# Kernel tuning notes

Hardware: AMD Instinct MI355X
Metric: run time of the kernel (lower is better)

Reference implementation:

```python
import jax, jax.numpy as jnp
import numpy as np

D_MODEL = 1024
N_HEADS = 16
D_FF = 512  # FeedForward default d_ff=512 (not overridden in EncoderLayer)
EPS = 1e-6


def _norm(x, alpha, bias):
    # Custom NormLayer: mean + UNBIASED variance (torch.var default, N-1 denom)
    mean = jnp.mean(x, axis=-1, keepdims=True)
    n = x.shape[-1]
    var = jnp.sum((x - mean) ** 2, axis=-1, keepdims=True) / (n - 1)
    return alpha * (x - mean) / jnp.sqrt(var + EPS) + bias


def setup_inputs() -> dict:
    key = jax.random.key(0)
    ks = jax.random.split(key, 12)
    s = 1.0 / np.sqrt(D_MODEL)
    inp = {
        "x": jax.random.normal(ks[0], (2, 2048, D_MODEL), dtype=jnp.float32),
        "Wq": jax.random.uniform(ks[1], (D_MODEL, D_MODEL), jnp.float32, -s, s),
        "bq": jnp.zeros((D_MODEL,), jnp.float32),
        "Wk": jax.random.uniform(ks[2], (D_MODEL, D_MODEL), jnp.float32, -s, s),
        "bk": jnp.zeros((D_MODEL,), jnp.float32),
        "Wv": jax.random.uniform(ks[3], (D_MODEL, D_MODEL), jnp.float32, -s, s),
        "bv": jnp.zeros((D_MODEL,), jnp.float32),
        "Wo": jax.random.uniform(ks[4], (D_MODEL, D_MODEL), jnp.float32, -s, s),
        "bo": jnp.zeros((D_MODEL,), jnp.float32),
        "alpha1": jnp.ones((D_MODEL,), jnp.float32),
        "beta1": jnp.zeros((D_MODEL,), jnp.float32),
        "alpha2": jnp.ones((D_MODEL,), jnp.float32),
        "beta2": jnp.zeros((D_MODEL,), jnp.float32),
        "W1": jax.random.uniform(ks[5], (D_MODEL, D_FF), jnp.float32, -s, s),
        "b1": jnp.zeros((D_FF,), jnp.float32),
        "W2": jax.random.uniform(ks[6], (D_FF, D_MODEL), jnp.float32, -1.0 / np.sqrt(D_FF), 1.0 / np.sqrt(D_FF)),
        "b2": jnp.zeros((D_MODEL,), jnp.float32),
    }
    return inp


def reference(x, Wq, bq, Wk, bk, Wv, bv, Wo, bo, alpha1, beta1, alpha2, beta2, W1, b1, W2, b2):
    B, S, D = x.shape
    H = N_HEADS
    dh = D // H
    # norm_1 applied to x, result feeds BOTH attention and the residual
    x = _norm(x, alpha1, beta1)
    # multihead attention (dropout = identity in eval)
    q = (x @ Wq + bq).reshape(B, S, H, dh)
    k = (x @ Wk + bk).reshape(B, S, H, dh)
    v = (x @ Wv + bv).reshape(B, S, H, dh)
    scores = jnp.einsum("bqhd,bkhd->bhqk", q, k) / jnp.sqrt(jnp.asarray(dh, x.dtype))
    attn = jax.nn.softmax(scores, axis=-1)
    o = jnp.einsum("bhqk,bkhd->bqhd", attn, v).reshape(B, S, D)
    o = o @ Wo + bo
    x = x + o
    # FFN on norm_2(x)
    h = _norm(x, alpha2, beta2)
    h = jax.nn.relu(h @ W1 + b1) @ W2 + b2
    return x + h
```

## Files before the change

kernel.cpp:

```cpp
#include <hip/hip_runtime.h>

typedef __bf16 bf16;
typedef __bf16 bf16x4 __attribute__((ext_vector_type(4)));
typedef __bf16 bf16x8 __attribute__((ext_vector_type(8)));
typedef float f32x4 __attribute__((ext_vector_type(4)));

#define D_MODEL 1024
#define SEQ 2048
#define NB 2
#define LOG2E 1.4426950408889634f

__device__ __forceinline__ void glds16(const bf16* g, bf16* l) {
    __builtin_amdgcn_global_load_lds(
        (const __attribute__((address_space(1))) void*)g,
        (__attribute__((address_space(3))) void*)l, 16, 0, 0);
}

__device__ __forceinline__ void tile_tcvt(
    const float* __restrict__ src, int rows, int cols, bf16* __restrict__ dst,
    int bx, int by, bf16 (*t)[72])
{
    int tid = threadIdx.x;
    int k0 = by * 64, n0 = bx * 64;
    int r = tid >> 2, c = (tid & 3) * 16;
    const float4* s = (const float4*)(src + (size_t)(k0 + r) * cols + n0 + c);
#pragma unroll
    for (int q = 0; q < 4; ++q) {
        float4 v = s[q];
        t[c + q * 4 + 0][r] = (bf16)v.x;
        t[c + q * 4 + 1][r] = (bf16)v.y;
        t[c + q * 4 + 2][r] = (bf16)v.z;
        t[c + q * 4 + 3][r] = (bf16)v.w;
    }
    __syncthreads();
    bf16* d = dst + (size_t)(n0 + r) * rows + k0 + c;
    *(bf16x8*)(d)     = *(const bf16x8*)&t[r][c];
    *(bf16x8*)(d + 8) = *(const bf16x8*)&t[r][c + 8];
}

__global__ __launch_bounds__(256) void prep_kernel(
    const float* __restrict__ Wq, const float* __restrict__ Wk,
    const float* __restrict__ Wv, const float* __restrict__ Wo,
    const float* __restrict__ W1, const float* __restrict__ W2,
    const float* __restrict__ bq, const float* __restrict__ bk,
    const float* __restrict__ bv,
    bf16* __restrict__ Wqkv_t, bf16* __restrict__ Wo_t,
    bf16* __restrict__ W1_t, bf16* __restrict__ W2_t,
    float* __restrict__ b_qkv)
{
    __shared__ bf16 t[64][72];
    int id = blockIdx.x;
    if (id < 1024) {
        int which = id >> 8, tile = id & 255;
        const float* src = which == 0 ? Wq : which == 1 ? Wk : which == 2 ? Wv : Wo;
        bf16* dst = which == 3 ? Wo_t : Wqkv_t + (size_t)which * 1024 * 1024;
        tile_tcvt(src, 1024, 1024, dst, tile & 15, tile >> 4, t);
    } else if (id < 1152) {
        int tile = id - 1024;
        tile_tcvt(W1, 1024, 512, W1_t, tile & 7, tile >> 3, t);
    } else if (id < 1280) {
        int tile = id - 1152;
        tile_tcvt(W2, 512, 1024, W2_t, tile & 15, tile >> 4, t);
    } else {
        int i = (id - 1280) * 256 + threadIdx.x;
        float v;
        if (i < 1024) v = bq[i];
        else if (i < 2048) v = bk[i - 1024];
        else v = bv[i - 2048];
        b_qkv[i] = v;
    }
}

__global__ __launch_bounds__(256) void norm_kernel(
    const float* __restrict__ X, const float* __restrict__ alpha,
    const float* __restrict__ beta, bf16* __restrict__ Y)
{
    int row = blockIdx.x;
    int tid = threadIdx.x;
    float4 v = ((const float4*)(X + (size_t)row * D_MODEL))[tid];
    float s = v.x + v.y + v.z + v.w;
    float ss = v.x*v.x + v.y*v.y + v.z*v.z + v.w*v.w;
#pragma unroll
    for (int off = 1; off < 64; off <<= 1) {
        s  += __shfl_xor(s, off, 64);
        ss += __shfl_xor(ss, off, 64);
    }
    __shared__ float sd[8];
    int wave = tid >> 6, lane = tid & 63;
    if (lane == 0) { sd[wave] = s; sd[4 + wave] = ss; }
    __syncthreads();
    s  = sd[0] + sd[1] + sd[2] + sd[3];
    ss = sd[4] + sd[5] + sd[6] + sd[7];
    float mean = s * (1.0f / 1024.0f);
    float var  = (ss - s * mean) * (1.0f / 1023.0f);
    float rs = rsqrtf(var + 1e-6f);
    float4 a = ((const float4*)alpha)[tid];
    float4 bt = ((const float4*)beta)[tid];
    bf16x4 o;
    o[0] = (bf16)(a.x * (v.x - mean) * rs + bt.x);
    o[1] = (bf16)(a.y * (v.y - mean) * rs + bt.y);
    o[2] = (bf16)(a.z * (v.z - mean) * rs + bt.z);
    o[3] = (bf16)(a.w * (v.w - mean) * rs + bt.w);
    *(bf16x4*)(Y + (size_t)row * D_MODEL + tid * 4) = o;
}

__global__ __launch_bounds__(256) void cnorm_kernel(
    const float* __restrict__ p0, const float* __restrict__ p1,
    const bf16* __restrict__ xn, const float* __restrict__ bo,
    const float* __restrict__ alpha, const float* __restrict__ beta,
    float* __restrict__ x2, bf16* __restrict__ hn)
{
    int row = blockIdx.x;
    int tid = threadIdx.x;
    float4 a = ((const float4*)(p0 + (size_t)row * D_MODEL))[tid];
    float4 b = ((const float4*)(p1 + (size_t)row * D_MODEL))[tid];
    float4 bb = ((const float4*)bo)[tid];
    bf16x4 xv = *(const bf16x4*)(xn + (size_t)row * D_MODEL + tid * 4);
    float4 v;
    v.x = a.x + b.x + bb.x + (float)xv[0];
    v.y = a.y + b.y + bb.y + (float)xv[1];
    v.z = a.z + b.z + bb.z + (float)xv[2];
    v.w = a.w + b.w + bb.w + (float)xv[3];
    ((float4*)(x2 + (size_t)row * D_MODEL))[tid] = v;
    float s = v.x + v.y + v.z + v.w;
    float ss = v.x*v.x + v.y*v.y + v.z*v.z + v.w*v.w;
#pragma unroll
    for (int off = 1; off < 64; off <<= 1) {
        s  += __shfl_xor(s, off, 64);
        ss += __shfl_xor(ss, off, 64);
    }
    __shared__ float sd[8];
    int wave = tid >> 6, lane = tid & 63;
    if (lane == 0) { sd[wave] = s; sd[4 + wave] = ss; }
    __syncthreads();
    s  = sd[0] + sd[1] + sd[2] + sd[3];
    ss = sd[4] + sd[5] + sd[6] + sd[7];
    float mean = s * (1.0f / 1024.0f);
    float var  = (ss - s * mean) * (1.0f / 1023.0f);
    float rs = rsqrtf(var + 1e-6f);
    float4 al = ((const float4*)alpha)[tid];
    float4 bt = ((const float4*)beta)[tid];
    bf16x4 o;
    o[0] = (bf16)(al.x * (v.x - mean) * rs + bt.x);
    o[1] = (bf16)(al.y * (v.y - mean) * rs + bt.y);
    o[2] = (bf16)(al.z * (v.z - mean) * rs + bt.z);
    o[3] = (bf16)(al.w * (v.w - mean) * rs + bt.w);
    *(bf16x4*)(hn + (size_t)row * D_MODEL + tid * 4) = o;
}

__global__ __launch_bounds__(256) void crelu_kernel(
    const float* __restrict__ p0, const float* __restrict__ p1,
    const float* __restrict__ b1, bf16* __restrict__ h1)
{
    int i = blockIdx.x * 256 + threadIdx.x;
    float4 a = ((const float4*)p0)[i];
    float4 b = ((const float4*)p1)[i];
    int col = (i * 4) & 511;
    float4 bb = *(const float4*)(b1 + col);
    bf16x4 o;
    o[0] = (bf16)fmaxf(a.x + b.x + bb.x, 0.0f);
    o[1] = (bf16)fmaxf(a.y + b.y + bb.y, 0.0f);
    o[2] = (bf16)fmaxf(a.z + b.z + bb.z, 0.0f);
    o[3] = (bf16)fmaxf(a.w + b.w + bb.w, 0.0f);
    ((bf16x4*)h1)[i] = o;
}

template <typename OutT, int BN, int KU, bool VFUSE, bool SPLITK>
__global__ __launch_bounds__(256) void gemm128(
    const bf16* __restrict__ A, const bf16* __restrict__ Bt,
    const float* __restrict__ bias, const float* __restrict__ Rf,
    OutT* __restrict__ C, bf16* __restrict__ vT,
    int M, int N, int K, int lda, int relu)
{
    constexpr int NT = BN / 32;
    constexpr int ASTR = 128 * 32;
    constexpr int BSTR = BN * 32;
    __shared__ bf16 As[ASTR * KU];
    __shared__ bf16 Bs[BSTR * KU];

    int tid = threadIdx.x;
    int wave = tid >> 6, lane = tid & 63;
    int quad = lane >> 4, l16 = lane & 15;
    int m0 = blockIdx.y * 128, n0 = blockIdx.x * BN;
    int wm = (wave >> 1) * 64, wn = (wave & 1) * (BN / 2);
    int Keff = SPLITK ? (K >> 1) : K;
    int klo  = SPLITK ? blockIdx.z * Keff : 0;

    f32x4 acc[4][NT] = {};

    const bf16* ga = A  + (size_t)(m0 + (tid >> 2)) * lda + (tid & 3) * 8 + klo;
    const bf16* gb = Bt + (size_t)(n0 + (tid >> 2)) * K   + (tid & 3) * 8 + klo;
    bf16* lAs = As + wave * 512;
    bf16* lBs = Bs + wave * 512;

    for (int k0 = 0; k0 < Keff; k0 += 32 * KU) {
        __syncthreads();
#pragma unroll
        for (int u = 0; u < KU; ++u) {
            glds16(ga + k0 + u * 32, lAs + u * ASTR);
            glds16(ga + (size_t)64 * lda + k0 + u * 32, lAs + u * ASTR + 2048);
            glds16(gb + k0 + u * 32, lBs + u * BSTR);
            if (BN == 128) glds16(gb + (size_t)64 * K + k0 + u * 32, lBs + u * BSTR + 2048);
        }
        __syncthreads();
#pragma unroll
        for (int u = 0; u < KU; ++u) {
            bf16x8 af[4], bfr[NT];
#pragma unroll
            for (int mt = 0; mt < 4; ++mt)
                af[mt] = *(const bf16x8*)(As + u * ASTR + (wm + mt * 16 + l16) * 32 + quad * 8);
#pragma unroll
            for (int nt = 0; nt < NT; ++nt)
                bfr[nt] = *(const bf16x8*)(Bs + u * BSTR + (wn + nt * 16 + l16) * 32 + quad * 8);
#pragma unroll
            for (int mt = 0; mt < 4; ++mt)
#pragma unroll
                for (int nt = 0; nt < NT; ++nt)
                    acc[mt][nt] = __builtin_amdgcn_mfma_f32_16x16x32_bf16(af[mt], bfr[nt], acc[mt][nt], 0, 0, 0);
        }
    }

    if (SPLITK) {
        float* P = (float*)C + (size_t)blockIdx.z * M * N;
#pragma unroll
        for (int nt = 0; nt < NT; ++nt) {
            int n = n0 + wn + nt * 16 + l16;
#pragma unroll
            for (int mt = 0; mt < 4; ++mt)
#pragma unroll
                for (int r = 0; r < 4; ++r) {
                    int m = m0 + wm + mt * 16 + quad * 4 + r;
                    P[(size_t)m * N + n] = acc[mt][nt][r];
                }
        }
        return;
    }

#pragma unroll
    for (int nt = 0; nt < NT; ++nt) {
        int n = n0 + wn + nt * 16 + l16;
        float bv = bias[n];
        if (VFUSE && n >= 2048) {
            int d = n & 63, h = (n - 2048) >> 6;
#pragma unroll
            for (int mt = 0; mt < 4; ++mt) {
                int m = m0 + wm + mt * 16 + quad * 4;
                int b = m >> 11, sidx = m & 2047;
                bf16x4 pk;
#pragma unroll
                for (int r = 0; r < 4; ++r) pk[r] = (bf16)(acc[mt][nt][r] + bv);
                *(bf16x4*)(vT + (((size_t)(b * 16 + h) * 64 + d) * SEQ + sidx)) = pk;
            }
        } else {
#pragma unroll
            for (int mt = 0; mt < 4; ++mt) {
#pragma unroll
                for (int r = 0; r < 4; ++r) {
                    int m = m0 + wm + mt * 16 + quad * 4 + r;
                    float vv = acc[mt][nt][r] + bv;
                    if (Rf) vv += Rf[(size_t)m * N + n];
                    if (relu) vv = vv > 0.0f ? vv : 0.0f;
                    C[(size_t)m * N + n] = (OutT)vv;
                }
            }
        }
    }
}

__global__ __launch_bounds__(256) void attn_kernel(
    const bf16* __restrict__ qkv, const bf16* __restrict__ vT, bf16* __restrict__ O)
{
    __shared__ bf16 Ks[64][72];
    __shared__ bf16 Vt[64][72];
    __shared__ bf16 Ps[4][32][72];

    int tid = threadIdx.x;
    int wave = tid >> 6, lane = tid & 63;
    int quad = lane >> 4, l16 = lane & 15;
    int bh = blockIdx.y, b = bh >> 4, h = bh & 15;
    int q0 = blockIdx.x * 128;

    const bf16* Qb = qkv + (size_t)(b * SEQ + q0 + wave * 32) * 3072 + h * 64;
    const bf16* Kb = qkv + (size_t)(b * SEQ) * 3072 + 1024 + h * 64;
    const bf16* Vb = vT + (size_t)bh * 64 * SEQ;

    const float c_l2 = 0.125f * LOG2E;
    bf16x8 qa[2][2];
#pragma unroll
    for (int mt = 0; mt < 2; ++mt)
#pragma unroll
        for (int hf = 0; hf < 2; ++hf) {
            bf16x8 raw = *(const bf16x8*)(Qb + (size_t)(mt * 16 + l16) * 3072 + hf * 32 + quad * 8);
            bf16x8 sc;
#pragma unroll
            for (int j = 0; j < 8; ++j) sc[j] = (bf16)((float)raw[j] * c_l2);
            qa[mt][hf] = sc;
        }

    float lsum[2] = {};
    f32x4 oacc[2][4] = {};

    int sr = tid >> 2, scol = (tid & 3) * 16;
    const bf16* kp = Kb + (size_t)sr * 3072 + scol;
    const bf16* vp = Vb + (size_t)sr * SEQ + scol;

    bf16x8 kr0 = ((const bf16x8*)kp)[0];
    bf16x8 kr1 = ((const bf16x8*)kp)[1];
    bf16x8 vr0 = ((const bf16x8*)vp)[0];
    bf16x8 vr1 = ((const bf16x8*)vp)[1];

    for (int kt = 0; kt < SEQ; kt += 64) {
        __syncthreads();
        *(bf16x8*)&Ks[sr][scol]     = kr0;
        *(bf16x8*)&Ks[sr][scol + 8] = kr1;
        *(bf16x8*)&Vt[sr][scol]     = vr0;
        *(bf16x8*)&Vt[sr][scol + 8] = vr1;
        __syncthreads();

        if (kt + 64 < SEQ) {
            const bf16* kn = kp + (size_t)(kt + 64) * 3072;
            const bf16* vn = vp + kt + 64;
            kr0 = ((const bf16x8*)kn)[0];
            kr1 = ((const bf16x8*)kn)[1];
            vr0 = ((const bf16x8*)vn)[0];
            vr1 = ((const bf16x8*)vn)[1];
        }

        bf16x8 kb[4][2];
#pragma unroll
        for (int t4 = 0; t4 < 4; ++t4) {
            kb[t4][0] = *(const bf16x8*)&Ks[t4 * 16 + l16][quad * 8];
            kb[t4][1] = *(const bf16x8*)&Ks[t4 * 16 + l16][32 + quad * 8];
        }
        bf16x8 vb[4][2];
#pragma unroll
        for (int dt = 0; dt < 4; ++dt) {
            vb[dt][0] = *(const bf16x8*)&Vt[dt * 16 + l16][quad * 8];
            vb[dt][1] = *(const bf16x8*)&Vt[dt * 16 + l16][32 + quad * 8];
        }
#pragma unroll
        for (int mt = 0; mt < 2; ++mt)
#pragma unroll
            for (int t4 = 0; t4 < 4; ++t4) {
                f32x4 c = {};
                c = __builtin_amdgcn_mfma_f32_16x16x32_bf16(kb[t4][0], qa[mt][0], c, 0, 0, 0);
                c = __builtin_amdgcn_mfma_f32_16x16x32_bf16(kb[t4][1], qa[mt][1], c, 0, 0, 0);
                bf16x4 pk;
                float psum = 0.0f;
#pragma unroll
                for (int r = 0; r < 4; ++r) {
                    float p = exp2f(c[r]);
                    psum += p;
                    pk[r] = (bf16)p;
                }
                lsum[mt] += psum;
                *(bf16x4*)&Ps[wave][mt * 16 + l16][t4 * 16 + quad * 4] = pk;
            }
#pragma unroll
        for (int mt = 0; mt < 2; ++mt) {
            bf16x8 pa0 = *(const bf16x8*)&Ps[wave][mt * 16 + l16][quad * 8];
            bf16x8 pa1 = *(const bf16x8*)&Ps[wave][mt * 16 + l16][32 + quad * 8];
#pragma unroll
            for (int dt = 0; dt < 4; ++dt) {
                oacc[mt][dt] = __builtin_amdgcn_mfma_f32_16x16x32_bf16(pa0, vb[dt][0], oacc[mt][dt], 0, 0, 0);
                oacc[mt][dt] = __builtin_amdgcn_mfma_f32_16x16x32_bf16(pa1, vb[dt][1], oacc[mt][dt], 0, 0, 0);
            }
        }
    }
#pragma unroll
    for (int mt = 0; mt < 2; ++mt) {
        float lr = lsum[mt];
        lr += __shfl_xor(lr, 16);
        lr += __shfl_xor(lr, 32);
#pragma unroll
        for (int r = 0; r < 4; ++r) {
            float inv = 1.0f / __shfl(lr, quad * 4 + r, 16);
            int row = b * SEQ + q0 + wave * 32 + mt * 16 + quad * 4 + r;
            bf16* op = O + (size_t)row * D_MODEL + h * 64;
#pragma unroll
            for (int dt = 0; dt < 4; ++dt)
                op[dt * 16 + l16] = (bf16)(oacc[mt][dt][r] * inv);
        }
    }
}

extern "C" void kernel_launch(void* const* d_in, const int* in_sizes, int n_in,
                              void* d_out, int out_size, void* d_ws, size_t ws_size,
                              hipStream_t stream)
{
    const float* x      = (const float*)d_in[0];
    const float* Wq     = (const float*)d_in[1];
    const float* bq     = (const float*)d_in[2];
    const float* Wk     = (const float*)d_in[3];
    const float* bk     = (const float*)d_in[4];
    const float* Wv     = (const float*)d_in[5];
    const float* bv     = (const float*)d_in[6];
    const float* Wo     = (const float*)d_in[7];
    const float* bo     = (const float*)d_in[8];
    const float* alpha1 = (const float*)d_in[9];
    const float* beta1  = (const float*)d_in[10];
    const float* alpha2 = (const float*)d_in[11];
    const float* beta2  = (const float*)d_in[12];
    const float* W1     = (const float*)d_in[13];
    const float* b1     = (const float*)d_in[14];
    const float* W2     = (const float*)d_in[15];
    const float* b2     = (const float*)d_in[16];

    char* ws = (char*)d_ws;
    const size_t MB = 1ull << 20;
    bf16*  Wqkv_t = (bf16*)(ws + 0 * MB);
    bf16*  Wo_t   = (bf16*)(ws + 6 * MB);
    bf16*  W1_t   = (bf16*)(ws + 8 * MB);
    bf16*  W2_t   = (bf16*)(ws + 9 * MB);
    float* b_qkv  = (float*)(ws + 10 * MB);
    bf16*  xn     = (bf16*)(ws + 11 * MB);
    bf16*  qkv    = (bf16*)(ws + 19 * MB);
    bf16*  vT     = (bf16*)(ws + 43 * MB);
    bf16*  o      = (bf16*)(ws + 51 * MB);
    float* pWo    = (float*)(ws + 19 * MB);
    float* x2     = (float*)(ws + 19 * MB);
    bf16*  hn     = (bf16*)(ws + 51 * MB);
    float* pF1    = (float*)(ws + 35 * MB);
    bf16*  h1     = (bf16*)(ws + 35 * MB);
    h1 = (bf16*)(ws + 55 * MB);
    h1 = (bf16*)(ws + 11 * MB);

    const int M = NB * SEQ;

    prep_kernel<<<1292, 256, 0, stream>>>(Wq, Wk, Wv, Wo, W1, W2, bq, bk, bv,
                                          Wqkv_t, Wo_t, W1_t, W2_t, b_qkv);

    norm_kernel<<<M, 256, 0, stream>>>(x, alpha1, beta1, xn);

    gemm128<bf16, 128, 2, true, false><<<dim3(24, 32), 256, 0, stream>>>(
        xn, Wqkv_t, b_qkv, nullptr, qkv, vT, M, 3072, D_MODEL, D_MODEL, 0);

    attn_kernel<<<dim3(SEQ / 128, 32), 256, 0, stream>>>(qkv, vT, o);

    gemm128<float, 128, 1, false, true><<<dim3(8, 32, 2), 256, 0, stream>>>(
        o, Wo_t, nullptr, nullptr, pWo, nullptr, M, D_MODEL, D_MODEL, D_MODEL, 0);

    cnorm_kernel<<<M, 256, 0, stream>>>(pWo, pWo + (size_t)M * D_MODEL, xn, bo,
                                        alpha2, beta2, x2, hn);

    gemm128<float, 64, 1, false, true><<<dim3(8, 32, 2), 256, 0, stream>>>(
        hn, W1_t, nullptr, nullptr, pF1, nullptr, M, 512, D_MODEL, D_MODEL, 0);

    crelu_kernel<<<(M * 512) / 1024, 256, 0, stream>>>(
        pF1, pF1 + (size_t)M * 512, b1, h1);

    gemm128<float, 64, 1, false, false><<<dim3(16, 32), 256, 0, stream>>>(
        h1, W2_t, b2, x2, (float*)d_out, nullptr, M, D_MODEL, 512, 512, 0);
}
```

Measured before the change: 283.2 us.

## Use 16-row waves in attention and fuse Wo residual epilogue

The attention kernel now runs 8 waves of 16 query rows each (512 threads) instead of 4 waves of 32 rows. Each thread stages one 8-element K/V chunk rather than two. This halves per-wave register state and spreads the K/V staging across more threads. Separately, the Wo projection drops split-K and switches to BN=64 tiles, adding bias and the bf16 residual in its epilogue, so the cnorm kernel is replaced by a plain norm_kernel over x2. This removes the split-K partial buffers and one elementwise pass, at the cost of each K/V tile now being reused by only 16 query rows per wave and less Wo GEMM parallelism.

```diff
diff --git a/kernel.cpp b/kernel.cpp
--- a/kernel.cpp
+++ b/kernel.cpp
@@ -104,50 +104,6 @@
     *(bf16x4*)(Y + (size_t)row * D_MODEL + tid * 4) = o;
 }
 
-__global__ __launch_bounds__(256) void cnorm_kernel(
-    const float* __restrict__ p0, const float* __restrict__ p1,
-    const bf16* __restrict__ xn, const float* __restrict__ bo,
-    const float* __restrict__ alpha, const float* __restrict__ beta,
-    float* __restrict__ x2, bf16* __restrict__ hn)
-{
-    int row = blockIdx.x;
-    int tid = threadIdx.x;
-    float4 a = ((const float4*)(p0 + (size_t)row * D_MODEL))[tid];
-    float4 b = ((const float4*)(p1 + (size_t)row * D_MODEL))[tid];
-    float4 bb = ((const float4*)bo)[tid];
-    bf16x4 xv = *(const bf16x4*)(xn + (size_t)row * D_MODEL + tid * 4);
-    float4 v;
-    v.x = a.x + b.x + bb.x + (float)xv[0];
-    v.y = a.y + b.y + bb.y + (float)xv[1];
-    v.z = a.z + b.z + bb.z + (float)xv[2];
-    v.w = a.w + b.w + bb.w + (float)xv[3];
-    ((float4*)(x2 + (size_t)row * D_MODEL))[tid] = v;
-    float s = v.x + v.y + v.z + v.w;
-    float ss = v.x*v.x + v.y*v.y + v.z*v.z + v.w*v.w;
-#pragma unroll
-    for (int off = 1; off < 64; off <<= 1) {
-        s  += __shfl_xor(s, off, 64);
-        ss += __shfl_xor(ss, off, 64);
-    }
-    __shared__ float sd[8];
-    int wave = tid >> 6, lane = tid & 63;
-    if (lane == 0) { sd[wave] = s; sd[4 + wave] = ss; }
-    __syncthreads();
-    s  = sd[0] + sd[1] + sd[2] + sd[3];
-    ss = sd[4] + sd[5] + sd[6] + sd[7];
-    float mean = s * (1.0f / 1024.0f);
-    float var  = (ss - s * mean) * (1.0f / 1023.0f);
-    float rs = rsqrtf(var + 1e-6f);
-    float4 al = ((const float4*)alpha)[tid];
-    float4 bt = ((const float4*)beta)[tid];
-    bf16x4 o;
-    o[0] = (bf16)(al.x * (v.x - mean) * rs + bt.x);
-    o[1] = (bf16)(al.y * (v.y - mean) * rs + bt.y);
-    o[2] = (bf16)(al.z * (v.z - mean) * rs + bt.z);
-    o[3] = (bf16)(al.w * (v.w - mean) * rs + bt.w);
-    *(bf16x4*)(hn + (size_t)row * D_MODEL + tid * 4) = o;
-}
-
 __global__ __launch_bounds__(256) void crelu_kernel(
     const float* __restrict__ p0, const float* __restrict__ p1,
     const float* __restrict__ b1, bf16* __restrict__ h1)
@@ -168,8 +124,8 @@
 template <typename OutT, int BN, int KU, bool VFUSE, bool SPLITK>
 __global__ __launch_bounds__(256) void gemm128(
     const bf16* __restrict__ A, const bf16* __restrict__ Bt,
-    const float* __restrict__ bias, const float* __restrict__ Rf,
-    OutT* __restrict__ C, bf16* __restrict__ vT,
+    const float* __restrict__ bias, const bf16* __restrict__ Rb,
+    const float* __restrict__ Rf, OutT* __restrict__ C, bf16* __restrict__ vT,
     int M, int N, int K, int lda, int relu)
 {
     constexpr int NT = BN / 32;
@@ -258,6 +214,7 @@
                 for (int r = 0; r < 4; ++r) {
                     int m = m0 + wm + mt * 16 + quad * 4 + r;
                     float vv = acc[mt][nt][r] + bv;
+                    if (Rb) vv += (float)Rb[(size_t)m * N + n];
                     if (Rf) vv += Rf[(size_t)m * N + n];
                     if (relu) vv = vv > 0.0f ? vv : 0.0f;
                     C[(size_t)m * N + n] = (OutT)vv;
@@ -267,12 +224,12 @@
     }
 }
 
-__global__ __launch_bounds__(256) void attn_kernel(
+__global__ __launch_bounds__(512) void attn_kernel(
     const bf16* __restrict__ qkv, const bf16* __restrict__ vT, bf16* __restrict__ O)
 {
     __shared__ bf16 Ks[64][72];
     __shared__ bf16 Vt[64][72];
-    __shared__ bf16 Ps[4][32][72];
+    __shared__ bf16 Ps[8][16][72];
 
     int tid = threadIdx.x;
     int wave = tid >> 6, lane = tid & 63;
@@ -280,107 +237,88 @@
     int bh = blockIdx.y, b = bh >> 4, h = bh & 15;
     int q0 = blockIdx.x * 128;
 
-    const bf16* Qb = qkv + (size_t)(b * SEQ + q0 + wave * 32) * 3072 + h * 64;
+    const bf16* Qb = qkv + (size_t)(b * SEQ + q0 + wave * 16) * 3072 + h * 64;
     const bf16* Kb = qkv + (size_t)(b * SEQ) * 3072 + 1024 + h * 64;
     const bf16* Vb = vT + (size_t)bh * 64 * SEQ;
 
     const float c_l2 = 0.125f * LOG2E;
-    bf16x8 qa[2][2];
-#pragma unroll
-    for (int mt = 0; mt < 2; ++mt)
-#pragma unroll
-        for (int hf = 0; hf < 2; ++hf) {
-            bf16x8 raw = *(const bf16x8*)(Qb + (size_t)(mt * 16 + l16) * 3072 + hf * 32 + quad * 8);
-            bf16x8 sc;
-#pragma unroll
-            for (int j = 0; j < 8; ++j) sc[j] = (bf16)((float)raw[j] * c_l2);
-            qa[mt][hf] = sc;
-        }
-
-    float lsum[2] = {};
-    f32x4 oacc[2][4] = {};
-
-    int sr = tid >> 2, scol = (tid & 3) * 16;
+    bf16x8 qa[2];
+#pragma unroll
+    for (int hf = 0; hf < 2; ++hf) {
+        bf16x8 raw = *(const bf16x8*)(Qb + (size_t)l16 * 3072 + hf * 32 + quad * 8);
+        bf16x8 sc;
+#pragma unroll
+        for (int j = 0; j < 8; ++j) sc[j] = (bf16)((float)raw[j] * c_l2);
+        qa[hf] = sc;
+    }
+
+    float lsum = 0.0f;
+    f32x4 oacc[4] = {};
+
+    int sr = tid >> 3, scol = (tid & 7) * 8;
     const bf16* kp = Kb + (size_t)sr * 3072 + scol;
     const bf16* vp = Vb + (size_t)sr * SEQ + scol;
 
-    bf16x8 kr0 = ((const bf16x8*)kp)[0];
-    bf16x8 kr1 = ((const bf16x8*)kp)[1];
-    bf16x8 vr0 = ((const bf16x8*)vp)[0];
-    bf16x8 vr1 = ((const bf16x8*)vp)[1];
+    bf16x8 kr = *(const bf16x8*)kp;
+    bf16x8 vr = *(const bf16x8*)vp;
 
     for (int kt = 0; kt < SEQ; kt += 64) {
         __syncthreads();
-        *(bf16x8*)&Ks[sr][scol]     = kr0;
-        *(bf16x8*)&Ks[sr][scol + 8] = kr1;
-        *(bf16x8*)&Vt[sr][scol]     = vr0;
-        *(bf16x8*)&Vt[sr][scol + 8] = vr1;
+        *(bf16x8*)&Ks[sr][scol] = kr;
+        *(bf16x8*)&Vt[sr][scol] = vr;
         __syncthreads();
 
         if (kt + 64 < SEQ) {
-            const bf16* kn = kp + (size_t)(kt + 64) * 3072;
-            const bf16* vn = vp + kt + 64;
-            kr0 = ((const bf16x8*)kn)[0];
-            kr1 = ((const bf16x8*)kn)[1];
-            vr0 = ((const bf16x8*)vn)[0];
-            vr1 = ((const bf16x8*)vn)[1];
-        }
-
-        bf16x8 kb[4][2];
+            kr = *(const bf16x8*)(kp + (size_t)(kt + 64) * 3072);
+            vr = *(const bf16x8*)(vp + kt + 64);
+        }
+
+        bf16x8 kb[4][2], vb[4][2];
 #pragma unroll
         for (int t4 = 0; t4 < 4; ++t4) {
             kb[t4][0] = *(const bf16x8*)&Ks[t4 * 16 + l16][quad * 8];
             kb[t4][1] = *(const bf16x8*)&Ks[t4 * 16 + l16][32 + quad * 8];
         }
-        bf16x8 vb[4][2];
 #pragma unroll
         for (int dt = 0; dt < 4; ++dt) {
             vb[dt][0] = *(const bf16x8*)&Vt[dt * 16 + l16][quad * 8];
             vb[dt][1] = *(const bf16x8*)&Vt[dt * 16 + l16][32 + quad * 8];
         }
 #pragma unroll
-        for (int mt = 0; mt < 2; ++mt)
-#pragma unroll
-            for (int t4 = 0; t4 < 4; ++t4) {
-                f32x4 c = {};
-                c = __builtin_amdgcn_mfma_f32_16x16x32_bf16(kb[t4][0], qa[mt][0], c, 0, 0, 0);
-                c = __builtin_amdgcn_mfma_f32_16x16x32_bf16(kb[t4][1], qa[mt][1], c, 0, 0, 0);
-                bf16x4 pk;
-                float psum = 0.0f;
-#pragma unroll
-                for (int r = 0; r < 4; ++r) {
-                    float p = exp2f(c[r]);
-                    psum += p;
-                    pk[r] = (bf16)p;
-                }
-                lsum[mt] += psum;
-                *(bf16x4*)&Ps[wave][mt * 16 + l16][t4 * 16 + quad * 4] = pk;
+        for (int t4 = 0; t4 < 4; ++t4) {
+            f32x4 c = {};
+            c = __builtin_amdgcn_mfma_f32_16x16x32_bf16(kb[t4][0], qa[0], c, 0, 0, 0);
+            c = __builtin_amdgcn_mfma_f32_16x16x32_bf16(kb[t4][1], qa[1], c, 0, 0, 0);
+            bf16x4 pk;
+            float psum = 0.0f;
+#pragma unroll
+            for (int r = 0; r < 4; ++r) {
+                float p = exp2f(c[r]);
+                psum += p;
+                pk[r] = (bf16)p;
             }
-#pragma unroll
-        for (int mt = 0; mt < 2; ++mt) {
-            bf16x8 pa0 = *(const bf16x8*)&Ps[wave][mt * 16 + l16][quad * 8];
-            bf16x8 pa1 = *(const bf16x8*)&Ps[wave][mt * 16 + l16][32 + quad * 8];
-#pragma unroll
-            for (int dt = 0; dt < 4; ++dt) {
-                oacc[mt][dt] = __builtin_amdgcn_mfma_f32_16x16x32_bf16(pa0, vb[dt][0], oacc[mt][dt], 0, 0, 0);
-                oacc[mt][dt] = __builtin_amdgcn_mfma_f32_16x16x32_bf16(pa1, vb[dt][1], oacc[mt][dt], 0, 0, 0);
-            }
-        }
-    }
-#pragma unroll
-    for (int mt = 0; mt < 2; ++mt) {
-        float lr = lsum[mt];
-        lr += __shfl_xor(lr, 16);
-        lr += __shfl_xor(lr, 32);
-#pragma unroll
-        for (int r = 0; r < 4; ++r) {
-            float inv = 1.0f / __shfl(lr, quad * 4 + r, 16);
-            int row = b * SEQ + q0 + wave * 32 + mt * 16 + quad * 4 + r;
-            bf16* op = O + (size_t)row * D_MODEL + h * 64;
-#pragma unroll
-            for (int dt = 0; dt < 4; ++dt)
-                op[dt * 16 + l16] = (bf16)(oacc[mt][dt][r] * inv);
-        }
+            lsum += psum;
+            *(bf16x4*)&Ps[wave][l16][t4 * 16 + quad * 4] = pk;
+        }
+        bf16x8 pa0 = *(const bf16x8*)&Ps[wave][l16][quad * 8];
+        bf16x8 pa1 = *(const bf16x8*)&Ps[wave][l16][32 + quad * 8];
+#pragma unroll
+        for (int dt = 0; dt < 4; ++dt) {
+            oacc[dt] = __builtin_amdgcn_mfma_f32_16x16x32_bf16(pa0, vb[dt][0], oacc[dt], 0, 0, 0);
+            oacc[dt] = __builtin_amdgcn_mfma_f32_16x16x32_bf16(pa1, vb[dt][1], oacc[dt], 0, 0, 0);
+        }
+    }
+    float lr = lsum;
+    lr += __shfl_xor(lr, 16);
+    lr += __shfl_xor(lr, 32);
+#pragma unroll
+    for (int r = 0; r < 4; ++r) {
+        float inv = 1.0f / __shfl(lr, quad * 4 + r, 16);
+        int row = b * SEQ + q0 + wave * 16 + quad * 4 + r;
+        bf16* op = O + (size_t)row * D_MODEL + h * 64;
+#pragma unroll
+        for (int dt = 0; dt < 4; ++dt)
+            op[dt * 16 + l16] = (bf16)(oacc[dt][r] * inv);
     }
 }
 
@@ -417,13 +355,10 @@
     bf16*  qkv    = (bf16*)(ws + 19 * MB);
     bf16*  vT     = (bf16*)(ws + 43 * MB);
     bf16*  o      = (bf16*)(ws + 51 * MB);
-    float* pWo    = (float*)(ws + 19 * MB);
     float* x2     = (float*)(ws + 19 * MB);
-    bf16*  hn     = (bf16*)(ws + 51 * MB);
-    float* pF1    = (float*)(ws + 35 * MB);
-    bf16*  h1     = (bf16*)(ws + 35 * MB);
-    h1 = (bf16*)(ws + 55 * MB);
-    h1 = (bf16*)(ws + 11 * MB);
+    bf16*  hn     = (bf16*)(ws + 35 * MB);
+    float* pF1    = (float*)(ws + 43 * MB);
+    bf16*  h1     = (bf16*)(ws + 11 * MB);
 
     const int M = NB * SEQ;
 
@@ -433,22 +368,21 @@
     norm_kernel<<<M, 256, 0, stream>>>(x, alpha1, beta1, xn);
 
     gemm128<bf16, 128, 2, true, false><<<dim3(24, 32), 256, 0, stream>>>(
-        xn, Wqkv_t, b_qkv, nullptr, qkv, vT, M, 3072, D_MODEL, D_MODEL, 0);
-
-    attn_kernel<<<dim3(SEQ / 128, 32), 256, 0, stream>>>(qkv, vT, o);
-
-    gemm128<float, 128, 1, false, true><<<dim3(8, 32, 2), 256, 0, stream>>>(
-        o, Wo_t, nullptr, nullptr, pWo, nullptr, M, D_MODEL, D_MODEL, D_MODEL, 0);
-
-    cnorm_kernel<<<M, 256, 0, stream>>>(pWo, pWo + (size_t)M * D_MODEL, xn, bo,
-                                        alpha2, beta2, x2, hn);
+        xn, Wqkv_t, b_qkv, nullptr, nullptr, qkv, vT, M, 3072, D_MODEL, D_MODEL, 0);
+
+    attn_kernel<<<dim3(SEQ / 128, 32), 512, 0, stream>>>(qkv, vT, o);
+
+    gemm128<float, 64, 1, false, false><<<dim3(16, 32), 256, 0, stream>>>(
+        o, Wo_t, bo, xn, nullptr, x2, nullptr, M, D_MODEL, D_MODEL, D_MODEL, 0);
+
+    norm_kernel<<<M, 256, 0, stream>>>(x2, alpha2, beta2, hn);
 
     gemm128<float, 64, 1, false, true><<<dim3(8, 32, 2), 256, 0, stream>>>(
-        hn, W1_t, nullptr, nullptr, pF1, nullptr, M, 512, D_MODEL, D_MODEL, 0);
+        hn, W1_t, nullptr, nullptr, nullptr, pF1, nullptr, M, 512, D_MODEL, D_MODEL, 0);
 
     crelu_kernel<<<(M * 512) / 1024, 256, 0, stream>>>(
         pF1, pF1 + (size_t)M * 512, b1, h1);
 
     gemm128<float, 64, 1, false, false><<<dim3(16, 32), 256, 0, stream>>>(
-        h1, W2_t, b2, x2, (float*)d_out, nullptr, M, D_MODEL, 512, 512, 0);
-}
+        h1, W2_t, b2, nullptr, x2, (float*)d_out, nullptr, M, D_MODEL, 512, 512, 0);
+}
```

After: 282.3 us. Within noise of the previous version (-0.3%).
